# Performance work log

Measured on AMD Instinct MI355X. Metric: run time of the kernel, lower is better.

## Reference

```python
import jax, jax.numpy as jnp
import numpy as np

B, N, D, E, H, HS = 2, 1024, 256, 64, 8, 64
FF = 4 * D
EPS = 1e-6


def _glorot(key, shape):
    fan_in, fan_out = shape[-2], shape[-1]
    lim = np.sqrt(6.0 / (fan_in + fan_out))
    return jax.random.uniform(key, shape, jnp.float32, -lim, lim)


def setup_inputs() -> dict:
    key = jax.random.key(0)
    ks = jax.random.split(key, 10)
    return {
        "node": jax.random.normal(ks[0], (B, N, D), jnp.float32),
        "edge": jax.random.normal(ks[1], (B, N, N, E), jnp.float32),
        "Wq": _glorot(ks[2], (H, D, HS)),
        "Wk": _glorot(ks[3], (H, D + E, HS)),
        "Wv": _glorot(ks[4], (H, D, HS)),
        "Wp": _glorot(ks[5], (H, HS, D)),
        "bp": jnp.zeros((D,), jnp.float32),
        "ln1_g": jnp.ones((D,), jnp.float32),
        "ln1_b": jnp.zeros((D,), jnp.float32),
        "W1": _glorot(ks[6], (D, FF)),
        "b1": jnp.zeros((FF,), jnp.float32),
        "W2": _glorot(ks[7], (FF, D)),
        "b2": jnp.zeros((D,), jnp.float32),
        "ln2_g": jnp.ones((D,), jnp.float32),
        "ln2_b": jnp.zeros((D,), jnp.float32),
    }


def _layernorm(x, g, b):
    mu = jnp.mean(x, axis=-1, keepdims=True)
    var = jnp.mean(jnp.square(x - mu), axis=-1, keepdims=True)
    return (x - mu) * jax.lax.rsqrt(var + EPS) * g + b


def reference(node, edge, Wq, Wk, Wv, Wp, bp, ln1_g, ln1_b, W1, b1, W2, b2, ln2_g, ln2_b):
    d_in = node.shape[-1]
    head_size = Wq.shape[-1]
    # query projection, scaled by sqrt(head_size)
    q = jnp.einsum('bni,hio->bnho', node, Wq) / jnp.sqrt(jnp.asarray(head_size, node.dtype))
    # key kernel split: node part [H, D, HS] and edge part [H, E, HS].
    # concat([repeat(key), edge]) @ Wk  ==  key @ Wk[:, :D] + edge @ Wk[:, D:]
    kn = jnp.einsum('bmi,hio->bmho', node, Wk[:, :d_in])          # [B,M,H,HS]
    logits = jnp.einsum('bnho,bmho->bhnm', q, kn)                 # node-key logits
    qe = jnp.einsum('bnho,heo->bnhe', q, Wk[:, d_in:])            # [B,N,H,E]
    logits = logits + jnp.einsum('bnhe,bnme->bhnm', qe, edge)     # edge-conditioned logits
    attn = jax.nn.softmax(logits, axis=-1)                        # [B,H,N,M]
    v = jnp.einsum('bmi,hio->bmho', node, Wv)                     # [B,M,H,HS]
    mo = jnp.einsum('bhnm,bmho->bnho', attn, v)                   # [B,N,H,HS]
    mha = jnp.einsum('bnhi,hio->bno', mo, Wp) + bp                # output projection
    # residual + layernorm (dropout = identity at eval)
    x = _layernorm(node + mha, ln1_g, ln1_b)
    # FFN: one hidden layer of ff_multi*D with relu, then project back to D
    ff = jax.nn.relu(x @ W1 + b1) @ W2 + b2
    return _layernorm(x + ff, ln2_g, ln2_b)
```

## Files before the change

### kernel.cpp

```cpp
#include <hip/hip_runtime.h>
#include <hip/hip_bf16.h>
#include <hip/hip_fp16.h>

#define B_  2
#define N_  1024
#define D_  256
#define E_  64
#define H_  8
#define HS_ 64
#define FF_ 1024
#define R_  (B_*N_)

typedef short bf8 __attribute__((ext_vector_type(8)));
typedef float f4  __attribute__((ext_vector_type(4)));

static __device__ __forceinline__ ushort f2b(float f) {
  __hip_bfloat16 h = __float2bfloat16(f);
  return *reinterpret_cast<ushort*>(&h);
}

static __device__ __forceinline__ ushort f2h(float f) {
  __half h = __float2half(f);
  return *reinterpret_cast<ushort*>(&h);
}

static __device__ __forceinline__ float h2f(ushort u) {
  __half h = *reinterpret_cast<__half*>(&u);
  return __half2float(h);
}

static __device__ __forceinline__ ushort4 f4_to_b4(float4 v) {
  ushort4 r;
  r.x = f2b(v.x); r.y = f2b(v.y); r.z = f2b(v.z); r.w = f2b(v.w);
  return r;
}

__global__ void k_pack(const float* __restrict__ node, const float* __restrict__ Wq,
                       const float* __restrict__ Wk, const float* __restrict__ Wv,
                       const float* __restrict__ Wp, const float* __restrict__ W1,
                       const float* __restrict__ W2,
                       ushort* __restrict__ node_bf, ushort* __restrict__ wqkvT,
                       ushort* __restrict__ wkeT, ushort* __restrict__ wpT,
                       ushort* __restrict__ w1T, ushort* __restrict__ w2T) {
  int idx = blockIdx.x * 256 + threadIdx.x;
  if (idx < 524288) {
    node_bf[idx] = f2b(node[idx]);
    return;
  }
  idx -= 524288;
  if (idx < 393216) {
    int c = idx >> 8, i = idx & 255;
    int mat = c >> 9, h = (c >> 6) & 7, o = c & 63;
    float v;
    if (mat == 0)      v = Wq[(h * 256 + i) * 64 + o] * 0.125f;
    else if (mat == 1) v = Wk[(h * 320 + i) * 64 + o];
    else               v = Wv[(h * 256 + i) * 64 + o];
    wqkvT[idx] = f2b(v);
    return;
  }
  idx -= 393216;
  if (idx < 262144) {
    int c = idx >> 9, r = idx & 511;
    int h2 = c >> 6, e = c & 63, h = r >> 6, o = r & 63;
    wkeT[idx] = (h2 == h) ? f2b(Wk[(h * 320 + 256 + e) * 64 + o]) : (ushort)0;
    return;
  }
  idx -= 262144;
  if (idx < 131072) {
    int c = idx >> 9, r = idx & 511;
    wpT[idx] = f2b(Wp[r * 256 + c]);
    return;
  }
  idx -= 131072;
  if (idx < 262144) {
    int c = idx >> 8, k = idx & 255;
    w1T[idx] = f2b(W1[k * 1024 + c]);
    return;
  }
  idx -= 262144;
  {
    int c = idx >> 10, k = idx & 1023;
    w2T[idx] = f2b(W2[k * 256 + c]);
  }
}

__global__ void k_vT(const ushort* __restrict__ qkv, ushort* __restrict__ vt) {
  int idx = blockIdx.x * 256 + threadIdx.x;
  if (idx >= 16 * 64 * 1024) return;
  int m = idx & 1023;
  int rest = idx >> 10;
  int o = rest & 63;
  int bh = rest >> 6;
  int b = bh >> 3, h = bh & 7;
  vt[idx] = qkv[(size_t)(b * 1024 + m) * 1536 + 1024 + h * 64 + o];
}

template<int EPI, int OFMT, int NBT, bool BDIAG>
__global__ void k_gemm(const ushort* __restrict__ A, const ushort* __restrict__ Bt,
                       void* __restrict__ Cv, const float* __restrict__ bias,
                       int M, int N, int K, int lda, int ldbt, int ldc,
                       long long as1, long long as2, long long bs1, long long bs2,
                       long long cs1, long long cs2) {
  int z = blockIdx.z;
  const ushort* Ab = A  + (size_t)((z >> 3) * as1 + (z & 7) * as2);
  const ushort* Bb = Bt + (size_t)((z >> 3) * bs1 + (z & 7) * bs2);
  size_t coff = (size_t)((z >> 3) * cs1 + (z & 7) * cs2);
  int r0 = blockIdx.x * 64, c0 = blockIdx.y * (64 * NBT);

  __shared__ ushort As[64][40];
  __shared__ ushort Bs[64 * NBT][40];

  int tid = threadIdx.x;
  int lane = tid & 63, w = tid >> 6;
  int wm = w >> 1, wn = w & 1;
  int kg = lane >> 4, lr = lane & 15;

  f4 acc[2][2 * NBT] = {};

  int kbeg = BDIAG ? c0 : 0;
  int kend = BDIAG ? c0 + 64 : K;
  for (int k0 = kbeg; k0 < kend; k0 += 32) {
    __syncthreads();
    {
      int row = tid >> 2, ch = tid & 3;
      *(int4*)&As[row][ch * 8] = *(const int4*)(Ab + (size_t)(r0 + row) * lda + k0 + ch * 8);
    }
    #pragma unroll
    for (int i = 0; i < NBT; ++i) {
      int row = (tid >> 2) + 64 * i, ch = tid & 3;
      *(int4*)&Bs[row][ch * 8] = *(const int4*)(Bb + (size_t)(c0 + row) * ldbt + k0 + ch * 8);
    }
    __syncthreads();

    bf8 bfr[2 * NBT];
    #pragma unroll
    for (int nt = 0; nt < NBT; ++nt)
      #pragma unroll
      for (int cb = 0; cb < 2; ++cb)
        bfr[nt * 2 + cb] = *(const bf8*)&Bs[nt * 64 + wn * 32 + cb * 16 + lr][kg * 8];
    #pragma unroll
    for (int rb = 0; rb < 2; ++rb) {
      bf8 af = *(const bf8*)&As[wm * 32 + rb * 16 + lr][kg * 8];
      #pragma unroll
      for (int q = 0; q < 2 * NBT; ++q)
        acc[rb][q] = __builtin_amdgcn_mfma_f32_16x16x32_bf16(af, bfr[q], acc[rb][q], 0, 0, 0);
    }
  }

  float*  Cf = (float*)Cv;
  ushort* Cb = (ushort*)Cv;
  __half* Ch = (__half*)Cv;
  #pragma unroll
  for (int rb = 0; rb < 2; ++rb) {
    #pragma unroll
    for (int q = 0; q < 2 * NBT; ++q) {
      #pragma unroll
      for (int rr = 0; rr < 4; ++rr) {
        int row = r0 + wm * 32 + rb * 16 + kg * 4 + rr;
        int col = c0 + (q >> 1) * 64 + wn * 32 + (q & 1) * 16 + lr;
        size_t ci = coff + (size_t)row * ldc + col;
        float v = acc[rb][q][rr];
        if (EPI >= 2) v += bias[col];
        if (EPI == 3) v = fmaxf(v, 0.0f);
        if (OFMT == 1)      Cb[ci] = f2b(v);
        else if (OFMT == 2) Ch[ci] = __float2half(v);
        else                Cf[ci] = v;
      }
    }
  }
}

__global__ __launch_bounds__(256, 4) void k_fused(
    const float* __restrict__ edge, const float* __restrict__ qe,
    const __half* __restrict__ logN, ushort* __restrict__ attn) {
  int bid = blockIdx.x;
  int b = bid >> 10, n = bid & 1023;
  int t = threadIdx.x;
  int lane = t & 63, w = t >> 6;
  int kg = lane >> 4, lr = lane & 15;

  __shared__ ushort As[128 * 64];
  __shared__ ushort lg[8][1032];
  __shared__ float red[2][4][8];

  bf8 bq[2];
  {
    const float* qrow = qe + (size_t)bid * 512 + (size_t)(lr & 7) * 64;
    #pragma unroll
    for (int kk = 0; kk < 2; ++kk) {
      float4 a  = *reinterpret_cast<const float4*>(&qrow[kk * 32 + kg * 8]);
      float4 c4 = *reinterpret_cast<const float4*>(&qrow[kk * 32 + kg * 8 + 4]);
      bq[kk][0] = (short)f2b(a.x);  bq[kk][1] = (short)f2b(a.y);
      bq[kk][2] = (short)f2b(a.z);  bq[kk][3] = (short)f2b(a.w);
      bq[kk][4] = (short)f2b(c4.x); bq[kk][5] = (short)f2b(c4.y);
      bq[kk][6] = (short)f2b(c4.z); bq[kk][7] = (short)f2b(c4.w);
    }
  }

  const float* eb = edge + (size_t)bid * 65536;

  float4 pf[8];
  #pragma unroll
  for (int u = 0; u < 8; ++u)
    pf[u] = reinterpret_cast<const float4*>(eb)[t + 256 * u];

  #pragma unroll 1
  for (int tl = 0; tl < 8; ++tl) {
    __syncthreads();
    #pragma unroll
    for (int u = 0; u < 8; ++u) {
      int g = t + 256 * u;
      int rl = g >> 4, c = t & 15;
      int slot = (c >> 1) ^ (rl & 7), half = c & 1;
      *reinterpret_cast<ushort4*>(&As[rl * 64 + slot * 8 + half * 4]) = f4_to_b4(pf[u]);
    }
    if (tl < 7) {
      const float4* src = reinterpret_cast<const float4*>(eb + (tl + 1) * 8192);
      #pragma unroll
      for (int u = 0; u < 8; ++u) pf[u] = src[t + 256 * u];
    }
    __syncthreads();

    #pragma unroll
    for (int sub = 0; sub < 2; ++sub) {
      int sr = w * 32 + sub * 16 + lr;
      f4 acc = {};
      #pragma unroll
      for (int kk = 0; kk < 2; ++kk) {
        bf8 af = *reinterpret_cast<const bf8*>(&As[sr * 64 + (((kk * 4 + kg) ^ (sr & 7)) << 3)]);
        acc = __builtin_amdgcn_mfma_f32_16x16x32_bf16(af, bq[kk], acc, 0, 0, 0);
      }
      if (lr < 8) {
        int mbase = tl * 128 + w * 32 + sub * 16 + kg * 4;
        uint2 pk;
        pk.x = (uint)f2h(acc[0]) | ((uint)f2h(acc[1]) << 16);
        pk.y = (uint)f2h(acc[2]) | ((uint)f2h(acc[3]) << 16);
        *reinterpret_cast<uint2*>(&lg[lr][mbase]) = pk;
      }
    }
  }

  ushort4 lNr[8];
  #pragma unroll
  for (int h = 0; h < 8; ++h)
    lNr[h] = *reinterpret_cast<const ushort4*>(
        &reinterpret_cast<const ushort*>(logN)[((size_t)(b * 8 + h) * 1024 + n) * 1024 + 4 * t]);
  __syncthreads();

  float l[4][8];
  #pragma unroll
  for (int h = 0; h < 8; ++h) {
    ushort4 lv = *reinterpret_cast<const ushort4*>(&lg[h][4 * t]);
    l[0][h] = h2f(lv.x) + h2f(lNr[h].x);
    l[1][h] = h2f(lv.y) + h2f(lNr[h].y);
    l[2][h] = h2f(lv.z) + h2f(lNr[h].z);
    l[3][h] = h2f(lv.w) + h2f(lNr[h].w);
  }
  float mx[8], sm[8];
  #pragma unroll
  for (int h = 0; h < 8; ++h) {
    float v = fmaxf(fmaxf(l[0][h], l[1][h]), fmaxf(l[2][h], l[3][h]));
    #pragma unroll
    for (int off = 32; off; off >>= 1) v = fmaxf(v, __shfl_xor(v, off));
    if (lane == 0) red[0][w][h] = v;
  }
  __syncthreads();
  #pragma unroll
  for (int h = 0; h < 8; ++h)
    mx[h] = fmaxf(fmaxf(red[0][0][h], red[0][1][h]), fmaxf(red[0][2][h], red[0][3][h]));
  #pragma unroll
  for (int j = 0; j < 4; ++j)
    #pragma unroll
    for (int h = 0; h < 8; ++h)
      l[j][h] = __expf(l[j][h] - mx[h]);
  #pragma unroll
  for (int h = 0; h < 8; ++h) {
    float v = l[0][h] + l[1][h] + l[2][h] + l[3][h];
    #pragma unroll
    for (int off = 32; off; off >>= 1) v += __shfl_xor(v, off);
    if (lane == 0) red[1][w][h] = v;
  }
  __syncthreads();
  #pragma unroll
  for (int h = 0; h < 8; ++h)
    sm[h] = 1.0f / (red[1][0][h] + red[1][1][h] + red[1][2][h] + red[1][3][h]);
  #pragma unroll
  for (int h = 0; h < 8; ++h) {
    size_t base = ((size_t)(b * 8 + h) * 1024 + n) * 1024;
    ushort4 o;
    o.x = f2b(l[0][h] * sm[h]);
    o.y = f2b(l[1][h] * sm[h]);
    o.z = f2b(l[2][h] * sm[h]);
    o.w = f2b(l[3][h] * sm[h]);
    *reinterpret_cast<ushort4*>(&attn[base + 4 * t]) = o;
  }
}

__global__ void k_ln(const float* __restrict__ a, const float* __restrict__ bb,
                     const float* __restrict__ g, const float* __restrict__ be,
                     float* __restrict__ of, ushort* __restrict__ ob) {
  int r = blockIdx.x, i = threadIdx.x;
  float t = a[(size_t)r * 256 + i] + bb[(size_t)r * 256 + i];
  __shared__ float red[4];

  float s = t;
  for (int off = 32; off; off >>= 1) s += __shfl_xor(s, off);
  if ((i & 63) == 0) red[i >> 6] = s;
  __syncthreads();
  float mean = (red[0] + red[1] + red[2] + red[3]) * (1.0f / 256.0f);
  __syncthreads();

  float d = t - mean;
  float q = d * d;
  for (int off = 32; off; off >>= 1) q += __shfl_xor(q, off);
  if ((i & 63) == 0) red[i >> 6] = q;
  __syncthreads();
  float var = (red[0] + red[1] + red[2] + red[3]) * (1.0f / 256.0f);

  float y = d * rsqrtf(var + 1e-6f) * g[i] + be[i];
  of[(size_t)r * 256 + i] = y;
  if (ob) ob[(size_t)r * 256 + i] = f2b(y);
}


extern "C" void kernel_launch(void* const* d_in, const int* in_sizes, int n_in,
                              void* d_out, int out_size, void* d_ws, size_t ws_size,
                              hipStream_t stream) {
  (void)in_sizes; (void)n_in; (void)out_size; (void)ws_size;
  const float* node = (const float*)d_in[0];
  const float* edge = (const float*)d_in[1];
  const float* Wq   = (const float*)d_in[2];
  const float* Wk   = (const float*)d_in[3];
  const float* Wv   = (const float*)d_in[4];
  const float* Wp   = (const float*)d_in[5];
  const float* bp   = (const float*)d_in[6];
  const float* g1   = (const float*)d_in[7];
  const float* be1  = (const float*)d_in[8];
  const float* W1   = (const float*)d_in[9];
  const float* b1   = (const float*)d_in[10];
  const float* W2   = (const float*)d_in[11];
  const float* b2   = (const float*)d_in[12];
  const float* g2   = (const float*)d_in[13];
  const float* be2  = (const float*)d_in[14];
  float* out = (float*)d_out;

  char* ws = (char*)d_ws;
  size_t off = 0;
  auto alloc = [&](size_t bytes) -> char* {
    char* p = ws + off;
    off = (off + bytes + 255) & ~(size_t)255;
    return p;
  };
  ushort* node_bf = (ushort*)alloc((size_t)R_ * D_ * 2);
  ushort* wqkvT   = (ushort*)alloc((size_t)1536 * 256 * 2);
  ushort* wkeT    = (ushort*)alloc((size_t)512 * 512 * 2);
  ushort* wpT     = (ushort*)alloc((size_t)256 * 512 * 2);
  ushort* w1T     = (ushort*)alloc((size_t)1024 * 256 * 2);
  ushort* w2T     = (ushort*)alloc((size_t)256 * 1024 * 2);
  ushort* qkv     = (ushort*)alloc((size_t)R_ * 1536 * 2);
  float*  qe      = (float*) alloc((size_t)R_ * 512 * 4);
  ushort* vt      = (ushort*)alloc((size_t)16 * 64 * 1024 * 2);
  __half* logits  = (__half*)alloc((size_t)16 * 1024 * 1024 * 2);
  ushort* attn    = (ushort*)alloc((size_t)16 * 1024 * 1024 * 2);
  ushort* mo      = (ushort*)alloc((size_t)R_ * 512 * 2);
  float*  mha     = (float*) alloc((size_t)R_ * 256 * 4);
  float*  xf      = (float*) alloc((size_t)R_ * 256 * 4);
  ushort* xb      = (ushort*)alloc((size_t)R_ * 256 * 2);
  ushort* hb      = (ushort*)alloc((size_t)R_ * 1024 * 2);
  float*  ff      = (float*) alloc((size_t)R_ * 256 * 4);

  k_pack<<<dim3(7168), dim3(256), 0, stream>>>(node, Wq, Wk, Wv, Wp, W1, W2,
                                               node_bf, wqkvT, wkeT, wpT, w1T, w2T);

  k_gemm<0, 1, 1, false><<<dim3(32, 24, 1), dim3(256), 0, stream>>>(
      node_bf, wqkvT, qkv, nullptr, 2048, 1536, 256, 256, 256, 1536,
      0LL, 0LL, 0LL, 0LL, 0LL, 0LL);

  k_gemm<0, 0, 1, true><<<dim3(32, 8, 1), dim3(256), 0, stream>>>(
      qkv, wkeT, qe, nullptr, 2048, 512, 512, 1536, 512, 512,
      0LL, 0LL, 0LL, 0LL, 0LL, 0LL);

  k_vT<<<dim3(4096), dim3(256), 0, stream>>>(qkv, vt);

  k_gemm<0, 2, 4, false><<<dim3(16, 4, 16), dim3(256), 0, stream>>>(
      qkv, qkv + 512, logits, nullptr, 1024, 1024, 64, 1536, 1536, 1024,
      1572864LL, 64LL, 1572864LL, 64LL, 8388608LL, 1048576LL);

  k_fused<<<dim3(2048), dim3(256), 0, stream>>>(edge, qe, logits, attn);

  k_gemm<0, 1, 1, false><<<dim3(16, 1, 16), dim3(256), 0, stream>>>(
      attn, vt, mo, nullptr, 1024, 64, 1024, 1024, 1024, 512,
      8388608LL, 1048576LL, 524288LL, 65536LL, 524288LL, 64LL);

  k_gemm<2, 0, 1, false><<<dim3(32, 4, 1), dim3(256), 0, stream>>>(
      mo, wpT, mha, bp, 2048, 256, 512, 512, 512, 256,
      0LL, 0LL, 0LL, 0LL, 0LL, 0LL);

  k_ln<<<dim3(2048), dim3(256), 0, stream>>>(node, mha, g1, be1, xf, xb);

  k_gemm<3, 1, 1, false><<<dim3(32, 16, 1), dim3(256), 0, stream>>>(
      xb, w1T, hb, b1, 2048, 1024, 256, 256, 256, 1024,
      0LL, 0LL, 0LL, 0LL, 0LL, 0LL);

  k_gemm<2, 0, 1, false><<<dim3(32, 4, 1), dim3(256), 0, stream>>>(
      hb, w2T, ff, b2, 2048, 256, 1024, 1024, 1024, 256,
      0LL, 0LL, 0LL, 0LL, 0LL, 0LL);

  k_ln<<<dim3(2048), dim3(256), 0, stream>>>(xf, ff, g2, be2, out, nullptr);
}
```

Before: 226.6 us.

## Load edge tiles directly into MFMA registers, drop LDS staging in fused attention

```diff
diff --git a/kernel.cpp b/kernel.cpp
--- a/kernel.cpp
+++ b/kernel.cpp
@@ -27,12 +27,6 @@
 static __device__ __forceinline__ float h2f(ushort u) {
   __half h = *reinterpret_cast<__half*>(&u);
   return __half2float(h);
-}
-
-static __device__ __forceinline__ ushort4 f4_to_b4(float4 v) {
-  ushort4 r;
-  r.x = f2b(v.x); r.y = f2b(v.y); r.z = f2b(v.z); r.w = f2b(v.w);
-  return r;
 }
 
 __global__ void k_pack(const float* __restrict__ node, const float* __restrict__ Wq,
@@ -170,7 +164,7 @@
   }
 }
 
-__global__ __launch_bounds__(256, 4) void k_fused(
+__global__ __launch_bounds__(256, 6) void k_fused(
     const float* __restrict__ edge, const float* __restrict__ qe,
     const __half* __restrict__ logN, ushort* __restrict__ attn) {
   int bid = blockIdx.x;
@@ -179,7 +173,6 @@
   int lane = t & 63, w = t >> 6;
   int kg = lane >> 4, lr = lane & 15;
 
-  __shared__ ushort As[128 * 64];
   __shared__ ushort lg[8][1032];
   __shared__ float red[2][4][8];
 
@@ -199,44 +192,28 @@
 
   const float* eb = edge + (size_t)bid * 65536;
 
-  float4 pf[8];
-  #pragma unroll
-  for (int u = 0; u < 8; ++u)
-    pf[u] = reinterpret_cast<const float4*>(eb)[t + 256 * u];
-
-  #pragma unroll 1
-  for (int tl = 0; tl < 8; ++tl) {
-    __syncthreads();
-    #pragma unroll
-    for (int u = 0; u < 8; ++u) {
-      int g = t + 256 * u;
-      int rl = g >> 4, c = t & 15;
-      int slot = (c >> 1) ^ (rl & 7), half = c & 1;
-      *reinterpret_cast<ushort4*>(&As[rl * 64 + slot * 8 + half * 4]) = f4_to_b4(pf[u]);
-    }
-    if (tl < 7) {
-      const float4* src = reinterpret_cast<const float4*>(eb + (tl + 1) * 8192);
-      #pragma unroll
-      for (int u = 0; u < 8; ++u) pf[u] = src[t + 256 * u];
-    }
-    __syncthreads();
-
-    #pragma unroll
-    for (int sub = 0; sub < 2; ++sub) {
-      int sr = w * 32 + sub * 16 + lr;
-      f4 acc = {};
-      #pragma unroll
-      for (int kk = 0; kk < 2; ++kk) {
-        bf8 af = *reinterpret_cast<const bf8*>(&As[sr * 64 + (((kk * 4 + kg) ^ (sr & 7)) << 3)]);
-        acc = __builtin_amdgcn_mfma_f32_16x16x32_bf16(af, bq[kk], acc, 0, 0, 0);
-      }
-      if (lr < 8) {
-        int mbase = tl * 128 + w * 32 + sub * 16 + kg * 4;
-        uint2 pk;
-        pk.x = (uint)f2h(acc[0]) | ((uint)f2h(acc[1]) << 16);
-        pk.y = (uint)f2h(acc[2]) | ((uint)f2h(acc[3]) << 16);
-        *reinterpret_cast<uint2*>(&lg[lr][mbase]) = pk;
-      }
+  #pragma unroll 4
+  for (int st = 0; st < 16; ++st) {
+    int sr = w * 256 + st * 16 + lr;
+    f4 acc = {};
+    #pragma unroll
+    for (int kk = 0; kk < 2; ++kk) {
+      const float* p = eb + (size_t)sr * 64 + kk * 32 + kg * 8;
+      float4 a  = *reinterpret_cast<const float4*>(p);
+      float4 c4 = *reinterpret_cast<const float4*>(p + 4);
+      bf8 af;
+      af[0] = (short)f2b(a.x);  af[1] = (short)f2b(a.y);
+      af[2] = (short)f2b(a.z);  af[3] = (short)f2b(a.w);
+      af[4] = (short)f2b(c4.x); af[5] = (short)f2b(c4.y);
+      af[6] = (short)f2b(c4.z); af[7] = (short)f2b(c4.w);
+      acc = __builtin_amdgcn_mfma_f32_16x16x32_bf16(af, bq[kk], acc, 0, 0, 0);
+    }
+    if (lr < 8) {
+      int mbase = w * 256 + st * 16 + kg * 4;
+      uint2 pk;
+      pk.x = (uint)f2h(acc[0]) | ((uint)f2h(acc[1]) << 16);
+      pk.y = (uint)f2h(acc[2]) | ((uint)f2h(acc[3]) << 16);
+      *reinterpret_cast<uint2*>(&lg[lr][mbase]) = pk;
     }
   }
 
```

Result: slower. 240.5 us (+6.1%).

## Fold edge-key projection into fused QKV GEMM via precomputed Wq·Wk_edge

Applied to the files above, without the earlier changes.

```diff
diff --git a/kernel.cpp b/kernel.cpp
--- a/kernel.cpp
+++ b/kernel.cpp
@@ -40,8 +40,8 @@
                        const float* __restrict__ Wp, const float* __restrict__ W1,
                        const float* __restrict__ W2,
                        ushort* __restrict__ node_bf, ushort* __restrict__ wqkvT,
-                       ushort* __restrict__ wkeT, ushort* __restrict__ wpT,
-                       ushort* __restrict__ w1T, ushort* __restrict__ w2T) {
+                       ushort* __restrict__ wpT, ushort* __restrict__ w1T,
+                       ushort* __restrict__ w2T, ushort* __restrict__ wqeT) {
   int idx = blockIdx.x * 256 + threadIdx.x;
   if (idx < 524288) {
     node_bf[idx] = f2b(node[idx]);
@@ -59,13 +59,6 @@
     return;
   }
   idx -= 393216;
-  if (idx < 262144) {
-    int c = idx >> 9, r = idx & 511;
-    int h2 = c >> 6, e = c & 63, h = r >> 6, o = r & 63;
-    wkeT[idx] = (h2 == h) ? f2b(Wk[(h * 320 + 256 + e) * 64 + o]) : (ushort)0;
-    return;
-  }
-  idx -= 262144;
   if (idx < 131072) {
     int c = idx >> 9, r = idx & 511;
     wpT[idx] = f2b(Wp[r * 256 + c]);
@@ -78,9 +71,21 @@
     return;
   }
   idx -= 262144;
-  {
+  if (idx < 262144) {
     int c = idx >> 10, k = idx & 1023;
     w2T[idx] = f2b(W2[k * 256 + c]);
+    return;
+  }
+  idx -= 262144;
+  {
+    int c = idx >> 8, i = idx & 255;
+    int h = c >> 6, e = c & 63;
+    const float* wq = Wq + (size_t)(h * 256 + i) * 64;
+    const float* we = Wk + (size_t)(h * 320 + 256 + e) * 64;
+    float s = 0.f;
+    #pragma unroll 8
+    for (int o = 0; o < 64; ++o) s += wq[o] * we[o];
+    wqeT[idx] = f2b(s * 0.125f);
   }
 }
 
@@ -92,10 +97,10 @@
   int o = rest & 63;
   int bh = rest >> 6;
   int b = bh >> 3, h = bh & 7;
-  vt[idx] = qkv[(size_t)(b * 1024 + m) * 1536 + 1024 + h * 64 + o];
-}
-
-template<int EPI, int OFMT, int NBT, bool BDIAG>
+  vt[idx] = qkv[(size_t)(b * 1024 + m) * 2048 + 1024 + h * 64 + o];
+}
+
+template<int EPI, int OFMT, int NBT>
 __global__ void k_gemm(const ushort* __restrict__ A, const ushort* __restrict__ Bt,
                        void* __restrict__ Cv, const float* __restrict__ bias,
                        int M, int N, int K, int lda, int ldbt, int ldc,
@@ -117,9 +122,7 @@
 
   f4 acc[2][2 * NBT] = {};
 
-  int kbeg = BDIAG ? c0 : 0;
-  int kend = BDIAG ? c0 + 64 : K;
-  for (int k0 = kbeg; k0 < kend; k0 += 32) {
+  for (int k0 = 0; k0 < K; k0 += 32) {
     __syncthreads();
     {
       int row = tid >> 2, ch = tid & 3;
@@ -171,7 +174,7 @@
 }
 
 __global__ __launch_bounds__(256, 4) void k_fused(
-    const float* __restrict__ edge, const float* __restrict__ qe,
+    const float* __restrict__ edge, const ushort* __restrict__ qe, int ldqe,
     const __half* __restrict__ logN, ushort* __restrict__ attn) {
   int bid = blockIdx.x;
   int b = bid >> 10, n = bid & 1023;
@@ -185,16 +188,9 @@
 
   bf8 bq[2];
   {
-    const float* qrow = qe + (size_t)bid * 512 + (size_t)(lr & 7) * 64;
-    #pragma unroll
-    for (int kk = 0; kk < 2; ++kk) {
-      float4 a  = *reinterpret_cast<const float4*>(&qrow[kk * 32 + kg * 8]);
-      float4 c4 = *reinterpret_cast<const float4*>(&qrow[kk * 32 + kg * 8 + 4]);
-      bq[kk][0] = (short)f2b(a.x);  bq[kk][1] = (short)f2b(a.y);
-      bq[kk][2] = (short)f2b(a.z);  bq[kk][3] = (short)f2b(a.w);
-      bq[kk][4] = (short)f2b(c4.x); bq[kk][5] = (short)f2b(c4.y);
-      bq[kk][6] = (short)f2b(c4.z); bq[kk][7] = (short)f2b(c4.w);
-    }
+    const ushort* qrow = qe + (size_t)bid * ldqe + (size_t)(lr & 7) * 64;
+    bq[0] = *reinterpret_cast<const bf8*>(&qrow[kg * 8]);
+    bq[1] = *reinterpret_cast<const bf8*>(&qrow[32 + kg * 8]);
   }
 
   const float* eb = edge + (size_t)bid * 65536;
@@ -352,13 +348,11 @@
     return p;
   };
   ushort* node_bf = (ushort*)alloc((size_t)R_ * D_ * 2);
-  ushort* wqkvT   = (ushort*)alloc((size_t)1536 * 256 * 2);
-  ushort* wkeT    = (ushort*)alloc((size_t)512 * 512 * 2);
+  ushort* wqkvBig = (ushort*)alloc((size_t)2048 * 256 * 2);
   ushort* wpT     = (ushort*)alloc((size_t)256 * 512 * 2);
   ushort* w1T     = (ushort*)alloc((size_t)1024 * 256 * 2);
   ushort* w2T     = (ushort*)alloc((size_t)256 * 1024 * 2);
-  ushort* qkv     = (ushort*)alloc((size_t)R_ * 1536 * 2);
-  float*  qe      = (float*) alloc((size_t)R_ * 512 * 4);
+  ushort* qkv     = (ushort*)alloc((size_t)R_ * 2048 * 2);
   ushort* vt      = (ushort*)alloc((size_t)16 * 64 * 1024 * 2);
   __half* logits  = (__half*)alloc((size_t)16 * 1024 * 1024 * 2);
   ushort* attn    = (ushort*)alloc((size_t)16 * 1024 * 1024 * 2);
@@ -369,40 +363,39 @@
   ushort* hb      = (ushort*)alloc((size_t)R_ * 1024 * 2);
   float*  ff      = (float*) alloc((size_t)R_ * 256 * 4);
 
-  k_pack<<<dim3(7168), dim3(256), 0, stream>>>(node, Wq, Wk, Wv, Wp, W1, W2,
-                                               node_bf, wqkvT, wkeT, wpT, w1T, w2T);
-
-  k_gemm<0, 1, 1, false><<<dim3(32, 24, 1), dim3(256), 0, stream>>>(
-      node_bf, wqkvT, qkv, nullptr, 2048, 1536, 256, 256, 256, 1536,
+  ushort* wqkvT = wqkvBig;
+  ushort* wqeT  = wqkvBig + (size_t)1536 * 256;
+
+  k_pack<<<dim3(6656), dim3(256), 0, stream>>>(node, Wq, Wk, Wv, Wp, W1, W2,
+                                               node_bf, wqkvT, wpT, w1T, w2T, wqeT);
+
+  k_gemm<0, 1, 1><<<dim3(32, 32, 1), dim3(256), 0, stream>>>(
+      node_bf, wqkvBig, qkv, nullptr, 2048, 2048, 256, 256, 256, 2048,
       0LL, 0LL, 0LL, 0LL, 0LL, 0LL);
 
-  k_gemm<0, 0, 1, true><<<dim3(32, 8, 1), dim3(256), 0, stream>>>(
-      qkv, wkeT, qe, nullptr, 2048, 512, 512, 1536, 512, 512,
-      0LL, 0LL, 0LL, 0LL, 0LL, 0LL);
-
   k_vT<<<dim3(4096), dim3(256), 0, stream>>>(qkv, vt);
 
-  k_gemm<0, 2, 4, false><<<dim3(16, 4, 16), dim3(256), 0, stream>>>(
-      qkv, qkv + 512, logits, nullptr, 1024, 1024, 64, 1536, 1536, 1024,
-      1572864LL, 64LL, 1572864LL, 64LL, 8388608LL, 1048576LL);
-
-  k_fused<<<dim3(2048), dim3(256), 0, stream>>>(edge, qe, logits, attn);
-
-  k_gemm<0, 1, 1, false><<<dim3(16, 1, 16), dim3(256), 0, stream>>>(
+  k_gemm<0, 2, 4><<<dim3(16, 4, 16), dim3(256), 0, stream>>>(
+      qkv, qkv + 512, logits, nullptr, 1024, 1024, 64, 2048, 2048, 1024,
+      2097152LL, 64LL, 2097152LL, 64LL, 8388608LL, 1048576LL);
+
+  k_fused<<<dim3(2048), dim3(256), 0, stream>>>(edge, qkv + 1536, 2048, logits, attn);
+
+  k_gemm<0, 1, 1><<<dim3(16, 1, 16), dim3(256), 0, stream>>>(
       attn, vt, mo, nullptr, 1024, 64, 1024, 1024, 1024, 512,
       8388608LL, 1048576LL, 524288LL, 65536LL, 524288LL, 64LL);
 
-  k_gemm<2, 0, 1, false><<<dim3(32, 4, 1), dim3(256), 0, stream>>>(
+  k_gemm<2, 0, 1><<<dim3(32, 4, 1), dim3(256), 0, stream>>>(
       mo, wpT, mha, bp, 2048, 256, 512, 512, 512, 256,
       0LL, 0LL, 0LL, 0LL, 0LL, 0LL);
 
   k_ln<<<dim3(2048), dim3(256), 0, stream>>>(node, mha, g1, be1, xf, xb);
 
-  k_gemm<3, 1, 1, false><<<dim3(32, 16, 1), dim3(256), 0, stream>>>(
+  k_gemm<3, 1, 1><<<dim3(32, 16, 1), dim3(256), 0, stream>>>(
       xb, w1T, hb, b1, 2048, 1024, 256, 256, 256, 1024,
       0LL, 0LL, 0LL, 0LL, 0LL, 0LL);
 
-  k_gemm<2, 0, 1, false><<<dim3(32, 4, 1), dim3(256), 0, stream>>>(
+  k_gemm<2, 0, 1><<<dim3(32, 4, 1), dim3(256), 0, stream>>>(
       hb, w2T, ff, b2, 2048, 256, 1024, 1024, 1024, 256,
       0LL, 0LL, 0LL, 0LL, 0LL, 0LL);
 
```

Result: slower. 236.1 us (+4.2%).
